# Kernel optimization log

Hardware: AMD Instinct MI355X
Metric: run time of the kernel (lower is better)

The kernel has to match this reference:

```python
import jax, jax.numpy as jnp
import numpy as np
from jax import lax


def fps(xyz, npoint, init_far):
    # Faithful farthest-point sampling: sequential loop over npoint iterations.
    B, N, _ = xyz.shape
    bidx = jnp.arange(B)

    def step(carry, _):
        dist, far = carry
        c = xyz[bidx, far]                       # (B,3) current centroid
        d = jnp.sum((xyz - c[:, None, :]) ** 2, -1)  # (B,N)
        dist = jnp.minimum(dist, d)
        return (dist, jnp.argmax(dist, -1)), far     # emit index BEFORE update, as in torch

    init = (jnp.full((B, N), 1e10, xyz.dtype), init_far)
    _, cent = lax.scan(step, init, None, length=npoint)  # (npoint, B)
    return cent.T                                         # (B, npoint)


def gather_pts(feat, idx):
    # feat (B,N,C), idx (B,K) -> (B,K,C)
    return jnp.take_along_axis(feat, idx[..., None], axis=1)


def setup_inputs() -> dict:
    key = jax.random.key(0)
    ks = jax.random.split(key, 12)
    B, N = 128, 500

    def w(k, o, i):
        return jax.random.normal(k, (o, i), jnp.float32) * 0.02

    z = lambda o: jnp.zeros((o,), jnp.float32)
    return {
        "x": jax.random.normal(ks[0], (B, N, 3), jnp.float32),
        "conf_W": w(ks[1], 1, 3),   "conf_b": z(1),
        "w1": w(ks[2], 64, 4),      "b1": z(64),
        "w2": w(ks[3], 256, 64),    "b2": z(256),
        "pc1_W": w(ks[4], 256, 256),"pc1_b": z(256),
        "w3": w(ks[5], 256, 259),   "b3": z(256),
        "w4": w(ks[6], 384, 256),   "b4": z(384),
        "pc2_W": w(ks[7], 384, 384),"pc2_b": z(384),
        "w5": w(ks[8], 384, 387),   "b5": z(384),
        "w6": w(ks[9], 512, 384),   "b6": z(512),
        "model_weights": 0,
        "init_far1": jax.random.randint(ks[10], (B,), 0, N),
        "init_far2": jax.random.randint(ks[11], (B,), 0, N),
    }


def reference(x, conf_W, conf_b, w1, b1, w2, b2, pc1_W, pc1_b,
              w3, b3, w4, b4, pc2_W, pc2_b, w5, b5, w6, b6,
              model_weights, init_far1, init_far2):
    relu = jax.nn.relu
    lin = lambda h, W, b: h @ W.T + b

    # ConfidenceScorePredictor: per-point sigmoid score (1 channel)
    conf = jax.nn.sigmoid(lin(x, conf_W, conf_b))            # (B,N,1)
    feat = jnp.concatenate([conf, x], -1)                    # (B,N,4)

    l2 = relu(lin(relu(lin(feat, w1, b1)), w2, b2))          # (B,N,256)
    l3 = lin(l2, pc1_W, pc1_b)                               # Conv1d k=1 == per-point linear

    idx1 = fps(x, 500, init_far1)                            # (B,500)
    nf1 = jnp.concatenate([gather_pts(l3, idx1), gather_pts(x, idx1)], -1)  # (B,500,259)

    l5 = relu(lin(relu(lin(nf1, w3, b3)), w4, b4))           # (B,500,384)
    l6 = lin(l5, pc2_W, pc2_b)                               # (B,500,384)

    idx2 = fps(x, 1000, init_far2)                           # (B,1000), indices < 500
    nf2 = jnp.concatenate([gather_pts(l6, idx2), gather_pts(x, idx2)], -1)  # (B,1000,387)

    l8 = relu(lin(relu(lin(nf2, w5, b5)), w6, b6))           # (B,1000,512)
    return jnp.max(l8, axis=1)                               # MaxPool1d(k=1000) -> (B,512)
```

## Files before the change

kernel.cpp:

```cpp
#include <hip/hip_runtime.h>

typedef unsigned short u16;
typedef short bf16x8 __attribute__((ext_vector_type(8)));
typedef float f32x4 __attribute__((ext_vector_type(4)));
typedef unsigned short us8 __attribute__((ext_vector_type(8)));
typedef unsigned long long u64;

__device__ __forceinline__ u16 f2bf(float f) {
  unsigned u = __float_as_uint(f);
  u += 0x7fffu + ((u >> 16) & 1u);
  return (u16)(u >> 16);
}

#define OFF_L6U 0u
#define OFF_IDX1 49152000u
#define OFF_FPSD 49408000u
#define OFF_FPSI 49670144u
#define OFF_WB   49671168u

template <int CTRL>
__device__ __forceinline__ unsigned dppu(unsigned v) {
  return (unsigned)__builtin_amdgcn_update_dpp(0, (int)v, CTRL, 0xF, 0xF, true);
}
template <int CTRL>
__device__ __forceinline__ float dppf(float v) {
  return __uint_as_float(dppu<CTRL>(__float_as_uint(v)));
}
__device__ __forceinline__ void ksel(u64& ak, float& ax, float& ay, float& az,
                                     u64 bk, float bx, float by, float bz) {
  bool g = bk > ak;
  ak = g ? bk : ak;
  ax = g ? bx : ax;
  ay = g ? by : ay;
  az = g ? bz : az;
}
template <int CTRL>
__device__ __forceinline__ void bstep_dpp(u64& k, float& x, float& y, float& z) {
  unsigned lo = (unsigned)k, hi = (unsigned)(k >> 32);
  unsigned olo = dppu<CTRL>(lo), ohi = dppu<CTRL>(hi);
  float ox = dppf<CTRL>(x), oy = dppf<CTRL>(y), oz = dppf<CTRL>(z);
  ksel(k, x, y, z, (((u64)ohi) << 32) | olo, ox, oy, oz);
}
__device__ __forceinline__ void bstep_shfl(int m, u64& k, float& x, float& y,
                                           float& z) {
  unsigned lo = (unsigned)k, hi = (unsigned)(k >> 32);
  unsigned olo = (unsigned)__shfl_xor((int)lo, m, 64);
  unsigned ohi = (unsigned)__shfl_xor((int)hi, m, 64);
  float ox = __shfl_xor(x, m, 64);
  float oy = __shfl_xor(y, m, 64);
  float oz = __shfl_xor(z, m, 64);
  ksel(k, x, y, z, (((u64)ohi) << 32) | olo, ox, oy, oz);
}

__device__ void fps_seg(const float4* cpt, int* out, const int* init1,
                        float* dstate, int* fstate, int b, int t0, int tcnt,
                        int lane) {
  __builtin_amdgcn_s_setprio(3);
  float px[8], py[8], pz[8], dist[8];
  unsigned nl[8];
  int base = lane * 8;
#pragma unroll
  for (int j = 0; j < 8; ++j) {
    int p = base + j;
    float4 c = cpt[p < 500 ? p : 0];
    px[j] = c.x; py[j] = c.y; pz[j] = c.z;
    nl[j] = ~(unsigned)p;
  }
  int fidx;
  if (t0 == 0) {
#pragma unroll
    for (int j = 0; j < 8; ++j) dist[j] = 1e10f;
    fidx = init1[b];
  } else {
#pragma unroll
    for (int j = 0; j < 8; ++j) dist[j] = dstate[(b * 64 + lane) * 8 + j];
    fidx = fstate[b];
  }
  float4 c0 = cpt[fidx];
  float cx = c0.x, cy = c0.y, cz = c0.z;

  int hist = 0;
  int tend = t0 + tcnt;
  for (int t = t0; t < tend; ++t) {
    hist = (lane == (t & 63)) ? fidx : hist;
    if ((t & 63) == 63) out[(t & ~63) + lane] = hist;
    if (t == 499) break;
#pragma unroll
    for (int j = 0; j < 8; ++j) {
      float dx = __fsub_rn(px[j], cx);
      float dy = __fsub_rn(py[j], cy);
      float dz = __fsub_rn(pz[j], cz);
      float d = __fadd_rn(__fadd_rn(__fmul_rn(dx, dx), __fmul_rn(dy, dy)),
                          __fmul_rn(dz, dz));
      dist[j] = fminf(dist[j], d);
    }
    u64 k[4];
    float X[4], Y[4], Z[4];
#pragma unroll
    for (int j = 0; j < 4; ++j) {
      u64 ka = (((u64)__float_as_uint(dist[2 * j])) << 32) | nl[2 * j];
      u64 kb = (((u64)__float_as_uint(dist[2 * j + 1])) << 32) | nl[2 * j + 1];
      bool g = kb > ka;
      k[j] = g ? kb : ka;
      X[j] = g ? px[2 * j + 1] : px[2 * j];
      Y[j] = g ? py[2 * j + 1] : py[2 * j];
      Z[j] = g ? pz[2 * j + 1] : pz[2 * j];
    }
    ksel(k[0], X[0], Y[0], Z[0], k[1], X[1], Y[1], Z[1]);
    ksel(k[2], X[2], Y[2], Z[2], k[3], X[3], Y[3], Z[3]);
    ksel(k[0], X[0], Y[0], Z[0], k[2], X[2], Y[2], Z[2]);
    bstep_dpp<0x121>(k[0], X[0], Y[0], Z[0]);
    bstep_dpp<0x122>(k[0], X[0], Y[0], Z[0]);
    bstep_dpp<0x124>(k[0], X[0], Y[0], Z[0]);
    bstep_dpp<0x128>(k[0], X[0], Y[0], Z[0]);
    bstep_shfl(16, k[0], X[0], Y[0], Z[0]);
    bstep_shfl(32, k[0], X[0], Y[0], Z[0]);
    fidx = (int)(~(unsigned)k[0]);
    cx = X[0]; cy = Y[0]; cz = Z[0];
  }
  if ((tend & 63) != 0) {
    int fb = (tend - 1) & ~63;
    if (lane <= ((tend - 1) & 63)) out[fb + lane] = hist;
  }
  if (tend < 500) {
#pragma unroll
    for (int j = 0; j < 8; ++j) dstate[(b * 64 + lane) * 8 + j] = dist[j];
    if (lane == 0) fstate[b] = fidx;
  }
}

template <int MI, int NI, int NP, int AG, int XC>
__device__ __forceinline__ void gemm_acc(
    f32x4 acc[MI][NI], const u16* __restrict__ aL, int Win, int smask,
    int arow0, const u16* const* aG, const u16* __restrict__ xc,
    const u16* __restrict__ bb, int Kp, int mrow, int quad) {
#pragma unroll
  for (int mi = 0; mi < MI; ++mi)
#pragma unroll
    for (int ni = 0; ni < NI; ++ni) acc[mi][ni] = f32x4{0.f, 0.f, 0.f, 0.f};
#pragma unroll
  for (int kp = 0; kp < NP + XC; ++kp) {
    bf16x8 af[MI];
#pragma unroll
    for (int mi = 0; mi < MI; ++mi) {
      int r = arow0 + mi * 16 + mrow;
      if (XC && kp == NP)
        af[mi] = *(const bf16x8*)(xc + r * 32 + ((quad ^ (r & 3)) << 3));
      else if (AG)
        af[mi] = *(const bf16x8*)(aG[mi] + kp * 32);
      else
        af[mi] = *(const bf16x8*)(aL + r * Win +
                                  (((kp * 4 + quad) ^ (r & smask)) << 3));
    }
    bf16x8 bf[NI];
#pragma unroll
    for (int ni = 0; ni < NI; ++ni)
      bf[ni] = *(const bf16x8*)(bb + (size_t)ni * 16 * Kp + kp * 32);
#pragma unroll
    for (int mi = 0; mi < MI; ++mi)
#pragma unroll
      for (int ni = 0; ni < NI; ++ni)
        acc[mi][ni] = __builtin_amdgcn_mfma_f32_16x16x32_bf16(
            af[mi], bf[ni], acc[mi][ni], 0, 0, 0);
  }
}

template <int MI, int NI>
__device__ __forceinline__ void ep_lds(const f32x4 acc[MI][NI], u16* out,
                                       int Wout, const float* __restrict__ bias,
                                       int n0, int arow0, int relu, int mrow,
                                       int quad) {
#pragma unroll
  for (int ni = 0; ni < NI; ++ni) {
    int col = n0 + ni * 16 + mrow;
    float bv = bias[col];
    int seg0 = col >> 3, lo = col & 7;
#pragma unroll
    for (int mi = 0; mi < MI; ++mi)
#pragma unroll
      for (int r = 0; r < 4; ++r) {
        int row = arow0 + mi * 16 + quad * 4 + r;
        float v = acc[mi][ni][r] + bv;
        if (relu) v = fmaxf(v, 0.f);
        out[row * Wout + ((seg0 ^ (row & 7)) << 3) + lo] = f2bf(v);
      }
  }
}

template <int MI, int NI>
__device__ __forceinline__ void ep_glb(const f32x4 acc[MI][NI],
                                       u16* __restrict__ out, int ldo,
                                       const float* __restrict__ bias, int n0,
                                       long grow0, long rowlim, int relu,
                                       int mrow, int quad) {
#pragma unroll
  for (int ni = 0; ni < NI; ++ni) {
    int col = n0 + ni * 16 + mrow;
    float bv = bias[col];
#pragma unroll
    for (int mi = 0; mi < MI; ++mi)
#pragma unroll
      for (int r = 0; r < 4; ++r) {
        long grow = grow0 + mi * 16 + quad * 4 + r;
        if (grow < rowlim) {
          float v = acc[mi][ni][r] + bv;
          if (relu) v = fmaxf(v, 0.f);
          out[(size_t)grow * ldo + col] = f2bf(v);
        }
      }
  }
}

struct ABArgs {
  const u16 *w1, *w2, *pc1, *w3, *w4, *pc2;
  const float *b1, *b2, *pc1b, *b3, *b4, *pc2b;
};

#define AB_LDS_BYTES (98304 + 8192)

__global__ __launch_bounds__(512, 2) void fused_ab(
    ABArgs A, const float* __restrict__ x, const float* __restrict__ cW,
    const float* __restrict__ cb, u16* __restrict__ l6u,
    const int* __restrict__ init1, int* __restrict__ idx1,
    float* __restrict__ dstate, int* __restrict__ fstate, int t0, int tcnt) {
  extern __shared__ __align__(16) char smem[];
  u16* act = (u16*)smem;
  u16* xcat = (u16*)(smem + 98304);
  int bid = blockIdx.x, t = threadIdx.x;
  if (bid < 128) {
    float4* cpt = (float4*)smem;
    const float* xb = x + (size_t)bid * 1500;
    for (int p = t; p < 500; p += 512)
      cpt[p] = make_float4(xb[p * 3], xb[p * 3 + 1], xb[p * 3 + 2], 0.f);
    __syncthreads();
    if (t < 64)
      fps_seg(cpt, idx1 + bid * 500, init1, dstate, fstate, bid, t0, tcnt, t);
    return;
  }
  const int blk = bid - 128;
  const size_t rows0 = (size_t)blk * 128;
  if (t < 128) {
    size_t gr = rows0 + t;
    float x0 = x[gr * 3], x1 = x[gr * 3 + 1], x2 = x[gr * 3 + 2];
    float z = x0 * cW[0] + x1 * cW[1] + x2 * cW[2] + cb[0];
    float conf = 1.0f / (1.0f + expf(-z));
    us8 fv;
    fv[0] = f2bf(conf); fv[1] = f2bf(x0); fv[2] = f2bf(x1); fv[3] = f2bf(x2);
    fv[4] = 0; fv[5] = 0; fv[6] = 0; fv[7] = 0;
    *(us8*)(act + t * 32 + ((t & 3) << 3)) = fv;
    us8 xv;
    xv[0] = fv[1]; xv[1] = fv[2]; xv[2] = fv[3];
    xv[3] = 0; xv[4] = 0; xv[5] = 0; xv[6] = 0; xv[7] = 0;
    *(us8*)(xcat + t * 32 + ((t & 3) << 3)) = xv;
  }
  if (t < 384) {
    us8 zz = {0, 0, 0, 0, 0, 0, 0, 0};
    int r = t / 3, s = 1 + t % 3;
    *(us8*)(act + r * 32 + ((s ^ (r & 3)) << 3)) = zz;
    *(us8*)(xcat + r * 32 + ((s ^ (r & 3)) << 3)) = zz;
  }
  __syncthreads();
  const int w = t >> 6, lane = t & 63, mrow = lane & 15, quad = lane >> 4;
  const int wm = w >> 2, wn = w & 3;
  const int arow0 = wm * 64;
  {
    f32x4 acc[4][1];
    const u16* bb = A.w1 + (size_t)(wn * 16 + mrow) * 32 + quad * 8;
    gemm_acc<4, 1, 1, 0, 0>(acc, act, 32, 3, arow0, nullptr, nullptr, bb, 32,
                            mrow, quad);
    __syncthreads();
    ep_lds<4, 1>(acc, act, 64, A.b1, wn * 16, arow0, 1, mrow, quad);
    __syncthreads();
  }
  {
    f32x4 acc[4][4];
    const u16* bb = A.w2 + (size_t)(wn * 64 + mrow) * 64 + quad * 8;
    gemm_acc<4, 4, 2, 0, 0>(acc, act, 64, 7, arow0, nullptr, nullptr, bb, 64,
                            mrow, quad);
    __syncthreads();
    ep_lds<4, 4>(acc, act, 256, A.b2, wn * 64, arow0, 1, mrow, quad);
    __syncthreads();
  }
  {
    f32x4 acc[4][4];
    const u16* bb = A.pc1 + (size_t)(wn * 64 + mrow) * 256 + quad * 8;
    gemm_acc<4, 4, 8, 0, 0>(acc, act, 256, 7, arow0, nullptr, nullptr, bb, 256,
                            mrow, quad);
    __syncthreads();
    ep_lds<4, 4>(acc, act, 256, A.pc1b, wn * 64, arow0, 0, mrow, quad);
    __syncthreads();
  }
  {
    f32x4 acc[4][4];
    const u16* bb = A.w3 + (size_t)(wn * 64 + mrow) * 288 + quad * 8;
    gemm_acc<4, 4, 8, 0, 1>(acc, act, 256, 7, arow0, nullptr, xcat, bb, 288,
                            mrow, quad);
    __syncthreads();
    ep_lds<4, 4>(acc, act, 256, A.b3, wn * 64, arow0, 1, mrow, quad);
    __syncthreads();
  }
  {
    f32x4 acc[4][6];
    const u16* bb = A.w4 + (size_t)(wn * 96 + mrow) * 256 + quad * 8;
    gemm_acc<4, 6, 8, 0, 0>(acc, act, 256, 7, arow0, nullptr, nullptr, bb, 256,
                            mrow, quad);
    __syncthreads();
    ep_lds<4, 6>(acc, act, 384, A.b4, wn * 96, arow0, 1, mrow, quad);
    __syncthreads();
  }
  {
    f32x4 acc[4][6];
    const u16* bb = A.pc2 + (size_t)(wn * 96 + mrow) * 384 + quad * 8;
    gemm_acc<4, 6, 12, 0, 0>(acc, act, 384, 7, arow0, nullptr, nullptr, bb,
                             384, mrow, quad);
    ep_glb<4, 6>(acc, l6u, 384, A.pc2b, wn * 96, (long)(rows0 + arow0), 64000,
                 0, mrow, quad);
  }
}

struct CArgs {
  const u16 *w5, *w6;
  const float *b5, *b6;
};

#define C_LDS_BYTES (98304 + 8192 + 2048)

__global__ __launch_bounds__(512, 2) void fused_c(
    CArgs C, const float* __restrict__ x, const u16* __restrict__ l6u,
    float* __restrict__ outf, const int* __restrict__ idx1) {
  extern __shared__ __align__(16) char smem[];
  u16* l7 = (u16*)smem;
  u16* xcat = (u16*)(smem + 98304);
  float* red = (float*)(smem + 98304 + 8192);
  int bid = blockIdx.x, t = threadIdx.x;
  const int b = bid >> 2, q = bid & 3;
  const int prow0 = q * 128;
  if (t < 128) {
    int p = prow0 + t, pe = p < 500 ? p : 0;
    const float* xp = x + ((size_t)b * 500 + pe) * 3;
    us8 xv;
    xv[0] = f2bf(xp[0]); xv[1] = f2bf(xp[1]); xv[2] = f2bf(xp[2]);
    xv[3] = 0; xv[4] = 0; xv[5] = 0; xv[6] = 0; xv[7] = 0;
    *(us8*)(xcat + t * 32 + ((t & 3) << 3)) = xv;
  }
  if (t < 384) {
    us8 zz = {0, 0, 0, 0, 0, 0, 0, 0};
    int r = t / 3, s = 1 + t % 3;
    *(us8*)(xcat + r * 32 + ((s ^ (r & 3)) << 3)) = zz;
  }
  __syncthreads();
  const int w = t >> 6, lane = t & 63, mrow = lane & 15, quad = lane >> 4;
  const int wm = w >> 2, wn = w & 3;
  const int arow0 = wm * 64;
  {
    const u16* aG[4];
#pragma unroll
    for (int mi = 0; mi < 4; ++mi) {
      int p = prow0 + arow0 + mi * 16 + mrow;
      int pe = p < 500 ? p : 0;
      int s = idx1[b * 500 + pe];
      aG[mi] = l6u + ((size_t)b * 500 + s) * 384 + quad * 8;
    }
    f32x4 acc[4][6];
    const u16* bb = C.w5 + (size_t)(wn * 96 + mrow) * 416 + quad * 8;
    gemm_acc<4, 6, 12, 1, 1>(acc, nullptr, 0, 0, arow0, aG, xcat, bb, 416,
                             mrow, quad);
    ep_lds<4, 6>(acc, l7, 384, C.b5, wn * 96, arow0, 1, mrow, quad);
  }
  __syncthreads();
  {
#pragma unroll
    for (int ph = 0; ph < 2; ++ph) {
      f32x4 acc[4][4];
      int n0 = ph * 256 + wn * 64;
      const u16* bb = C.w6 + (size_t)(n0 + mrow) * 384 + quad * 8;
      gemm_acc<4, 4, 12, 0, 0>(acc, l7, 384, 7, arow0, nullptr, nullptr, bb,
                               384, mrow, quad);
#pragma unroll
      for (int ni = 0; ni < 4; ++ni) {
        int cc = n0 + ni * 16 + mrow;
        float bv = C.b6[cc];
        float mx = 0.f;
#pragma unroll
        for (int mi = 0; mi < 4; ++mi)
#pragma unroll
          for (int r = 0; r < 4; ++r) {
            int p = prow0 + arow0 + mi * 16 + quad * 4 + r;
            float v = fmaxf(acc[mi][ni][r] + bv, 0.f);
            if (p < 500) mx = fmaxf(mx, v);
          }
        mx = fmaxf(mx, __shfl_xor(mx, 16, 64));
        mx = fmaxf(mx, __shfl_xor(mx, 32, 64));
        if (quad == 0) red[wm * 256 + wn * 64 + ni * 16 + mrow] = mx;
      }
      __syncthreads();
      if (t < 256) {
        float m = fmaxf(red[t], red[256 + t]);
        atomicMax((unsigned*)&outf[(size_t)b * 512 + ph * 256 + t],
                  __float_as_uint(m));
      }
      __syncthreads();
    }
  }
}

struct PrepArgs {
  const float* wsrc[8];
  u16* wdst[8];
  int wN[8], wK[8], wKp[8];
  int wstart[9];
};

__global__ __launch_bounds__(256) void prep_kernel(
    PrepArgs pa, const float* __restrict__ x, float* __restrict__ outf,
    const int* __restrict__ init1, int* __restrict__ idx1,
    float* __restrict__ dstate, int* __restrict__ fstate, int tcnt) {
  __shared__ float4 cpt[512];
  int bid = blockIdx.x, t = threadIdx.x;
  if (bid < 128) {
    const float* xb = x + (size_t)bid * 1500;
    for (int p = t; p < 500; p += 256)
      cpt[p] = make_float4(xb[p * 3], xb[p * 3 + 1], xb[p * 3 + 2], 0.f);
    __syncthreads();
    if (t < 64)
      fps_seg(cpt, idx1 + bid * 500, init1, dstate, fstate, bid, 0, tcnt, t);
    return;
  }
  int i = (bid - 128) * 256 + t;
  int S = pa.wstart[8];
  if (i < S) {
    int wsel = 0;
#pragma unroll
    for (int j = 1; j < 8; ++j)
      if (i >= pa.wstart[j]) wsel = j;
    int local = i - pa.wstart[wsel];
    int Kp = pa.wKp[wsel];
    int n = local / Kp, k = local - n * Kp;
    pa.wdst[wsel][local] =
        (k < pa.wK[wsel]) ? f2bf(pa.wsrc[wsel][n * pa.wK[wsel] + k]) : (u16)0;
  } else if (i < S + 65536) {
    outf[i - S] = 0.f;
  }
}

extern "C" void kernel_launch(void* const* d_in, const int* in_sizes, int n_in,
                              void* d_out, int out_size, void* d_ws,
                              size_t ws_size, hipStream_t stream) {
  const float* x      = (const float*)d_in[0];
  const float* conf_W = (const float*)d_in[1];
  const float* conf_b = (const float*)d_in[2];
  const float* w1     = (const float*)d_in[3];
  const float* b1     = (const float*)d_in[4];
  const float* w2     = (const float*)d_in[5];
  const float* b2     = (const float*)d_in[6];
  const float* pc1_W  = (const float*)d_in[7];
  const float* pc1_b  = (const float*)d_in[8];
  const float* w3     = (const float*)d_in[9];
  const float* b3     = (const float*)d_in[10];
  const float* w4     = (const float*)d_in[11];
  const float* b4     = (const float*)d_in[12];
  const float* pc2_W  = (const float*)d_in[13];
  const float* pc2_b  = (const float*)d_in[14];
  const float* w5     = (const float*)d_in[15];
  const float* b5     = (const float*)d_in[16];
  const float* w6     = (const float*)d_in[17];
  const float* b6     = (const float*)d_in[18];
  const int* init1    = (const int*)d_in[20];

  char* ws = (char*)d_ws;
  u16* l6u = (u16*)(ws + OFF_L6U);
  int* idx1 = (int*)(ws + OFF_IDX1);
  float* dstate = (float*)(ws + OFF_FPSD);
  int* fstate = (int*)(ws + OFF_FPSI);
  u16* wb = (u16*)(ws + OFF_WB);
  float* outf = (float*)d_out;

  PrepArgs pa;
  const float* srcs[8] = {w1, w2, pc1_W, w3, w4, pc2_W, w5, w6};
  int Ns[8]  = {64, 256, 256, 256, 384, 384, 384, 512};
  int Ks[8]  = {4, 64, 256, 259, 256, 384, 387, 384};
  int Kps[8] = {32, 64, 256, 288, 256, 384, 416, 384};
  u16* WBp[8];
  int cum = 0;
  for (int i = 0; i < 8; ++i) {
    pa.wsrc[i] = srcs[i];
    pa.wdst[i] = WBp[i] = wb + cum;
    pa.wN[i] = Ns[i];
    pa.wK[i] = Ks[i];
    pa.wKp[i] = Kps[i];
    pa.wstart[i] = cum;
    cum += Ns[i] * Kps[i];
  }
  pa.wstart[8] = cum;
  int total = cum + 65536;

  prep_kernel<<<128 + (total + 255) / 256, 256, 0, stream>>>(
      pa, x, outf, init1, idx1, dstate, fstate, 64);

  ABArgs A;
  A.w1 = WBp[0]; A.w2 = WBp[1]; A.pc1 = WBp[2];
  A.w3 = WBp[3]; A.w4 = WBp[4]; A.pc2 = WBp[5];
  A.b1 = b1; A.b2 = b2; A.pc1b = pc1_b; A.b3 = b3; A.b4 = b4; A.pc2b = pc2_b;
  fused_ab<<<128 + 500, 512, AB_LDS_BYTES, stream>>>(
      A, x, conf_W, conf_b, l6u, init1, idx1, dstate, fstate, 64, 436);

  CArgs Cg;
  Cg.w5 = WBp[6]; Cg.w6 = WBp[7]; Cg.b5 = b5; Cg.b6 = b6;
  fused_c<<<512, 512, C_LDS_BYTES, stream>>>(Cg, x, l6u, outf, idx1);
}
```

Before: 471.5 us.

## Fold w5 GEMM into stage AB, simplify FPS argmax, pack two FPS batches per block

The w5 layer is now applied per source point inside fused_ab, before the gather, and its fp32 result is written to a larger workspace. fused_c then gathers those rows, adds the xyz term from the last three w5 columns in fp32 and applies relu, which removes the w5 GEMM from the gathered 1000-point stage. The FPS argmax changes from a 64-bit key-plus-coordinate butterfly to a float max reduction followed by a ballot to find the first matching index, and two batches' FPS now run in one block. The price is a doubled fp32 intermediate buffer and extra gather traffic in fused_c, and the w5 pre-activation now comes from bf16 GEMM on l6 instead of on gathered rows.

Result: faster. 408.0 us (-13.5%).

```diff
diff --git a/kernel.cpp b/kernel.cpp
--- a/kernel.cpp
+++ b/kernel.cpp
@@ -4,6 +4,7 @@
 typedef short bf16x8 __attribute__((ext_vector_type(8)));
 typedef float f32x4 __attribute__((ext_vector_type(4)));
 typedef unsigned short us8 __attribute__((ext_vector_type(8)));
+typedef unsigned short us4 __attribute__((ext_vector_type(4)));
 typedef unsigned long long u64;
 
 __device__ __forceinline__ u16 f2bf(float f) {
@@ -11,45 +12,20 @@
   u += 0x7fffu + ((u >> 16) & 1u);
   return (u16)(u >> 16);
 }
-
-#define OFF_L6U 0u
-#define OFF_IDX1 49152000u
-#define OFF_FPSD 49408000u
-#define OFF_FPSI 49670144u
-#define OFF_WB   49671168u
+__device__ __forceinline__ float rlf(float v, int l) {
+  return __uint_as_float((unsigned)__builtin_amdgcn_readlane(__float_as_int(v), l));
+}
+
+#define OFF_AP   0u
+#define OFF_IDX1 98304000u
+#define OFF_FPSD 98560000u
+#define OFF_FPSI 98822144u
+#define OFF_WB   98824192u
 
 template <int CTRL>
-__device__ __forceinline__ unsigned dppu(unsigned v) {
-  return (unsigned)__builtin_amdgcn_update_dpp(0, (int)v, CTRL, 0xF, 0xF, true);
-}
-template <int CTRL>
-__device__ __forceinline__ float dppf(float v) {
-  return __uint_as_float(dppu<CTRL>(__float_as_uint(v)));
-}
-__device__ __forceinline__ void ksel(u64& ak, float& ax, float& ay, float& az,
-                                     u64 bk, float bx, float by, float bz) {
-  bool g = bk > ak;
-  ak = g ? bk : ak;
-  ax = g ? bx : ax;
-  ay = g ? by : ay;
-  az = g ? bz : az;
-}
-template <int CTRL>
-__device__ __forceinline__ void bstep_dpp(u64& k, float& x, float& y, float& z) {
-  unsigned lo = (unsigned)k, hi = (unsigned)(k >> 32);
-  unsigned olo = dppu<CTRL>(lo), ohi = dppu<CTRL>(hi);
-  float ox = dppf<CTRL>(x), oy = dppf<CTRL>(y), oz = dppf<CTRL>(z);
-  ksel(k, x, y, z, (((u64)ohi) << 32) | olo, ox, oy, oz);
-}
-__device__ __forceinline__ void bstep_shfl(int m, u64& k, float& x, float& y,
-                                           float& z) {
-  unsigned lo = (unsigned)k, hi = (unsigned)(k >> 32);
-  unsigned olo = (unsigned)__shfl_xor((int)lo, m, 64);
-  unsigned ohi = (unsigned)__shfl_xor((int)hi, m, 64);
-  float ox = __shfl_xor(x, m, 64);
-  float oy = __shfl_xor(y, m, 64);
-  float oz = __shfl_xor(z, m, 64);
-  ksel(k, x, y, z, (((u64)ohi) << 32) | olo, ox, oy, oz);
+__device__ __forceinline__ float dppmaxf(float v) {
+  int s = __builtin_amdgcn_update_dpp(0, __float_as_int(v), CTRL, 0xF, 0xF, true);
+  return fmaxf(v, __uint_as_float((unsigned)s));
 }
 
 __device__ void fps_seg(const float4* cpt, int* out, const int* init1,
@@ -57,14 +33,12 @@
                         int lane) {
   __builtin_amdgcn_s_setprio(3);
   float px[8], py[8], pz[8], dist[8];
-  unsigned nl[8];
   int base = lane * 8;
 #pragma unroll
   for (int j = 0; j < 8; ++j) {
     int p = base + j;
     float4 c = cpt[p < 500 ? p : 0];
     px[j] = c.x; py[j] = c.y; pz[j] = c.z;
-    nl[j] = ~(unsigned)p;
   }
   int fidx;
   if (t0 == 0) {
@@ -94,29 +68,30 @@
                           __fmul_rn(dz, dz));
       dist[j] = fminf(dist[j], d);
     }
-    u64 k[4];
-    float X[4], Y[4], Z[4];
-#pragma unroll
-    for (int j = 0; j < 4; ++j) {
-      u64 ka = (((u64)__float_as_uint(dist[2 * j])) << 32) | nl[2 * j];
-      u64 kb = (((u64)__float_as_uint(dist[2 * j + 1])) << 32) | nl[2 * j + 1];
-      bool g = kb > ka;
-      k[j] = g ? kb : ka;
-      X[j] = g ? px[2 * j + 1] : px[2 * j];
-      Y[j] = g ? py[2 * j + 1] : py[2 * j];
-      Z[j] = g ? pz[2 * j + 1] : pz[2 * j];
-    }
-    ksel(k[0], X[0], Y[0], Z[0], k[1], X[1], Y[1], Z[1]);
-    ksel(k[2], X[2], Y[2], Z[2], k[3], X[3], Y[3], Z[3]);
-    ksel(k[0], X[0], Y[0], Z[0], k[2], X[2], Y[2], Z[2]);
-    bstep_dpp<0x121>(k[0], X[0], Y[0], Z[0]);
-    bstep_dpp<0x122>(k[0], X[0], Y[0], Z[0]);
-    bstep_dpp<0x124>(k[0], X[0], Y[0], Z[0]);
-    bstep_dpp<0x128>(k[0], X[0], Y[0], Z[0]);
-    bstep_shfl(16, k[0], X[0], Y[0], Z[0]);
-    bstep_shfl(32, k[0], X[0], Y[0], Z[0]);
-    fidx = (int)(~(unsigned)k[0]);
-    cx = X[0]; cy = Y[0]; cz = Z[0];
+    float t1 = fmaxf(fmaxf(dist[0], dist[1]), dist[2]);
+    float t2 = fmaxf(fmaxf(dist[3], dist[4]), dist[5]);
+    float t3 = fmaxf(fmaxf(dist[6], dist[7]), t1);
+    float m = fmaxf(t2, t3);
+    m = dppmaxf<0x111>(m);
+    m = dppmaxf<0x112>(m);
+    m = dppmaxf<0x114>(m);
+    m = dppmaxf<0x118>(m);
+    m = dppmaxf<0x142>(m);
+    m = dppmaxf<0x143>(m);
+    float mf = rlf(m, 63);
+    int e0 = (dist[0] == mf) ? 0 : 8, e1 = (dist[1] == mf) ? 1 : 8;
+    int e2 = (dist[2] == mf) ? 2 : 8, e3 = (dist[3] == mf) ? 3 : 8;
+    int e4 = (dist[4] == mf) ? 4 : 8, e5 = (dist[5] == mf) ? 5 : 8;
+    int e6 = (dist[6] == mf) ? 6 : 8, e7 = (dist[7] == mf) ? 7 : 8;
+    int sA = min(min(e0, e1), e2);
+    int sB = min(min(e3, e4), e5);
+    int sC = min(min(e6, e7), sA);
+    int sel = min(sB, sC);
+    u64 mask = __ballot(sel != 8);
+    int li = (int)__ffsll(mask) - 1;
+    fidx = li * 8 + __builtin_amdgcn_readlane(sel, li);
+    float4 cc = cpt[fidx];
+    cx = cc.x; cy = cc.y; cz = cc.z;
   }
   if ((tend & 63) != 0) {
     int fb = (tend - 1) & ~63;
@@ -129,11 +104,11 @@
   }
 }
 
-template <int MI, int NI, int NP, int AG, int XC>
+template <int MI, int NI, int NP, int XC>
 __device__ __forceinline__ void gemm_acc(
     f32x4 acc[MI][NI], const u16* __restrict__ aL, int Win, int smask,
-    int arow0, const u16* const* aG, const u16* __restrict__ xc,
-    const u16* __restrict__ bb, int Kp, int mrow, int quad) {
+    int arow0, const u16* __restrict__ xc, const u16* __restrict__ bb, int Kp,
+    int mrow, int quad) {
 #pragma unroll
   for (int mi = 0; mi < MI; ++mi)
 #pragma unroll
@@ -146,8 +121,6 @@
       int r = arow0 + mi * 16 + mrow;
       if (XC && kp == NP)
         af[mi] = *(const bf16x8*)(xc + r * 32 + ((quad ^ (r & 3)) << 3));
-      else if (AG)
-        af[mi] = *(const bf16x8*)(aG[mi] + kp * 32);
       else
         af[mi] = *(const bf16x8*)(aL + r * Win +
                                   (((kp * 4 + quad) ^ (r & smask)) << 3));
@@ -188,11 +161,11 @@
 }
 
 template <int MI, int NI>
-__device__ __forceinline__ void ep_glb(const f32x4 acc[MI][NI],
-                                       u16* __restrict__ out, int ldo,
-                                       const float* __restrict__ bias, int n0,
-                                       long grow0, long rowlim, int relu,
-                                       int mrow, int quad) {
+__device__ __forceinline__ void ep_glbf(const f32x4 acc[MI][NI],
+                                        float* __restrict__ out, int ldo,
+                                        const float* __restrict__ bias, int n0,
+                                        long grow0, long rowlim, int mrow,
+                                        int quad) {
 #pragma unroll
   for (int ni = 0; ni < NI; ++ni) {
     int col = n0 + ni * 16 + mrow;
@@ -202,42 +175,43 @@
 #pragma unroll
       for (int r = 0; r < 4; ++r) {
         long grow = grow0 + mi * 16 + quad * 4 + r;
-        if (grow < rowlim) {
-          float v = acc[mi][ni][r] + bv;
-          if (relu) v = fmaxf(v, 0.f);
-          out[(size_t)grow * ldo + col] = f2bf(v);
-        }
+        if (grow < rowlim)
+          out[(size_t)grow * ldo + col] = acc[mi][ni][r] + bv;
       }
   }
 }
 
 struct ABArgs {
-  const u16 *w1, *w2, *pc1, *w3, *w4, *pc2;
-  const float *b1, *b2, *pc1b, *b3, *b4, *pc2b;
+  const u16 *w1, *w2, *pc1, *w3, *w4, *pc2, *w5;
+  const float *b1, *b2, *pc1b, *b3, *b4, *pc2b, *b5;
 };
 
 #define AB_LDS_BYTES (98304 + 8192)
 
 __global__ __launch_bounds__(512, 2) void fused_ab(
     ABArgs A, const float* __restrict__ x, const float* __restrict__ cW,
-    const float* __restrict__ cb, u16* __restrict__ l6u,
+    const float* __restrict__ cb, float* __restrict__ apart,
     const int* __restrict__ init1, int* __restrict__ idx1,
     float* __restrict__ dstate, int* __restrict__ fstate, int t0, int tcnt) {
   extern __shared__ __align__(16) char smem[];
   u16* act = (u16*)smem;
   u16* xcat = (u16*)(smem + 98304);
   int bid = blockIdx.x, t = threadIdx.x;
-  if (bid < 128) {
+  if (bid < 64) {
     float4* cpt = (float4*)smem;
-    const float* xb = x + (size_t)bid * 1500;
-    for (int p = t; p < 500; p += 512)
+    const float* xb = x + (size_t)bid * 3000;
+    for (int p = t; p < 1000; p += 512)
       cpt[p] = make_float4(xb[p * 3], xb[p * 3 + 1], xb[p * 3 + 2], 0.f);
     __syncthreads();
-    if (t < 64)
-      fps_seg(cpt, idx1 + bid * 500, init1, dstate, fstate, bid, t0, tcnt, t);
+    int wid = t >> 6;
+    if (wid < 2) {
+      int b = bid * 2 + wid;
+      fps_seg(cpt + wid * 500, idx1 + b * 500, init1, dstate, fstate, b, t0,
+              tcnt, t & 63);
+    }
     return;
   }
-  const int blk = bid - 128;
+  const int blk = bid - 64;
   const size_t rows0 = (size_t)blk * 128;
   if (t < 128) {
     size_t gr = rows0 + t;
@@ -266,8 +240,7 @@
   {
     f32x4 acc[4][1];
     const u16* bb = A.w1 + (size_t)(wn * 16 + mrow) * 32 + quad * 8;
-    gemm_acc<4, 1, 1, 0, 0>(acc, act, 32, 3, arow0, nullptr, nullptr, bb, 32,
-                            mrow, quad);
+    gemm_acc<4, 1, 1, 0>(acc, act, 32, 3, arow0, nullptr, bb, 32, mrow, quad);
     __syncthreads();
     ep_lds<4, 1>(acc, act, 64, A.b1, wn * 16, arow0, 1, mrow, quad);
     __syncthreads();
@@ -275,8 +248,7 @@
   {
     f32x4 acc[4][4];
     const u16* bb = A.w2 + (size_t)(wn * 64 + mrow) * 64 + quad * 8;
-    gemm_acc<4, 4, 2, 0, 0>(acc, act, 64, 7, arow0, nullptr, nullptr, bb, 64,
-                            mrow, quad);
+    gemm_acc<4, 4, 2, 0>(acc, act, 64, 7, arow0, nullptr, bb, 64, mrow, quad);
     __syncthreads();
     ep_lds<4, 4>(acc, act, 256, A.b2, wn * 64, arow0, 1, mrow, quad);
     __syncthreads();
@@ -284,8 +256,7 @@
   {
     f32x4 acc[4][4];
     const u16* bb = A.pc1 + (size_t)(wn * 64 + mrow) * 256 + quad * 8;
-    gemm_acc<4, 4, 8, 0, 0>(acc, act, 256, 7, arow0, nullptr, nullptr, bb, 256,
-                            mrow, quad);
+    gemm_acc<4, 4, 8, 0>(acc, act, 256, 7, arow0, nullptr, bb, 256, mrow, quad);
     __syncthreads();
     ep_lds<4, 4>(acc, act, 256, A.pc1b, wn * 64, arow0, 0, mrow, quad);
     __syncthreads();
@@ -293,8 +264,7 @@
   {
     f32x4 acc[4][4];
     const u16* bb = A.w3 + (size_t)(wn * 64 + mrow) * 288 + quad * 8;
-    gemm_acc<4, 4, 8, 0, 1>(acc, act, 256, 7, arow0, nullptr, xcat, bb, 288,
-                            mrow, quad);
+    gemm_acc<4, 4, 8, 1>(acc, act, 256, 7, arow0, xcat, bb, 288, mrow, quad);
     __syncthreads();
     ep_lds<4, 4>(acc, act, 256, A.b3, wn * 64, arow0, 1, mrow, quad);
     __syncthreads();
@@ -302,8 +272,7 @@
   {
     f32x4 acc[4][6];
     const u16* bb = A.w4 + (size_t)(wn * 96 + mrow) * 256 + quad * 8;
-    gemm_acc<4, 6, 8, 0, 0>(acc, act, 256, 7, arow0, nullptr, nullptr, bb, 256,
-                            mrow, quad);
+    gemm_acc<4, 6, 8, 0>(acc, act, 256, 7, arow0, nullptr, bb, 256, mrow, quad);
     __syncthreads();
     ep_lds<4, 6>(acc, act, 384, A.b4, wn * 96, arow0, 1, mrow, quad);
     __syncthreads();
@@ -311,75 +280,81 @@
   {
     f32x4 acc[4][6];
     const u16* bb = A.pc2 + (size_t)(wn * 96 + mrow) * 384 + quad * 8;
-    gemm_acc<4, 6, 12, 0, 0>(acc, act, 384, 7, arow0, nullptr, nullptr, bb,
-                             384, mrow, quad);
-    ep_glb<4, 6>(acc, l6u, 384, A.pc2b, wn * 96, (long)(rows0 + arow0), 64000,
-                 0, mrow, quad);
-  }
-}
-
-struct CArgs {
-  const u16 *w5, *w6;
-  const float *b5, *b6;
-};
-
-#define C_LDS_BYTES (98304 + 8192 + 2048)
+    gemm_acc<4, 6, 12, 0>(acc, act, 384, 7, arow0, nullptr, bb, 384, mrow,
+                          quad);
+    __syncthreads();
+    ep_lds<4, 6>(acc, act, 384, A.pc2b, wn * 96, arow0, 0, mrow, quad);
+    __syncthreads();
+  }
+  {
+    f32x4 acc[4][6];
+    const u16* bb = A.w5 + (size_t)(wn * 96 + mrow) * 416 + quad * 8;
+    gemm_acc<4, 6, 12, 0>(acc, act, 384, 7, arow0, nullptr, bb, 416, mrow,
+                          quad);
+    ep_glbf<4, 6>(acc, apart, 384, A.b5, wn * 96, (long)(rows0 + arow0), 64000,
+                  mrow, quad);
+  }
+}
+
+#define C_LDS_BYTES (98304 + 6144 + 2048)
 
 __global__ __launch_bounds__(512, 2) void fused_c(
-    CArgs C, const float* __restrict__ x, const u16* __restrict__ l6u,
-    float* __restrict__ outf, const int* __restrict__ idx1) {
+    const u16* __restrict__ w6b, const float* __restrict__ b6,
+    const float* __restrict__ x, const float* __restrict__ apart,
+    const float* __restrict__ w5src, float* __restrict__ outf,
+    const int* __restrict__ idx1) {
   extern __shared__ __align__(16) char smem[];
   u16* l7 = (u16*)smem;
-  u16* xcat = (u16*)(smem + 98304);
-  float* red = (float*)(smem + 98304 + 8192);
+  float* xw = (float*)(smem + 98304);
+  float* red = (float*)(smem + 98304 + 6144);
   int bid = blockIdx.x, t = threadIdx.x;
   const int b = bid >> 2, q = bid & 3;
   const int prow0 = q * 128;
-  if (t < 128) {
-    int p = prow0 + t, pe = p < 500 ? p : 0;
+  if (t < 384) {
+    xw[t * 4 + 0] = w5src[(size_t)t * 387 + 384];
+    xw[t * 4 + 1] = w5src[(size_t)t * 387 + 385];
+    xw[t * 4 + 2] = w5src[(size_t)t * 387 + 386];
+    xw[t * 4 + 3] = 0.f;
+  }
+  __syncthreads();
+  {
+    int row = t >> 2;
+    int p = prow0 + row, pe = p < 500 ? p : 0;
+    int s = idx1[b * 500 + pe];
+    const float* ap = apart + ((size_t)b * 500 + (size_t)s) * 384;
     const float* xp = x + ((size_t)b * 500 + pe) * 3;
-    us8 xv;
-    xv[0] = f2bf(xp[0]); xv[1] = f2bf(xp[1]); xv[2] = f2bf(xp[2]);
-    xv[3] = 0; xv[4] = 0; xv[5] = 0; xv[6] = 0; xv[7] = 0;
-    *(us8*)(xcat + t * 32 + ((t & 3) << 3)) = xv;
-  }
-  if (t < 384) {
-    us8 zz = {0, 0, 0, 0, 0, 0, 0, 0};
-    int r = t / 3, s = 1 + t % 3;
-    *(us8*)(xcat + r * 32 + ((s ^ (r & 3)) << 3)) = zz;
+    float x0 = xp[0], x1 = xp[1], x2 = xp[2];
+#pragma unroll
+    for (int it = 0; it < 24; ++it) {
+      int c = (t & 3) * 4 + it * 16;
+      float4 a4 = *(const float4*)(ap + c);
+      const float4* wv = (const float4*)(xw + c * 4);
+      float v0 = fmaxf(a4.x + wv[0].x * x0 + wv[0].y * x1 + wv[0].z * x2, 0.f);
+      float v1 = fmaxf(a4.y + wv[1].x * x0 + wv[1].y * x1 + wv[1].z * x2, 0.f);
+      float v2 = fmaxf(a4.z + wv[2].x * x0 + wv[2].y * x1 + wv[2].z * x2, 0.f);
+      float v3 = fmaxf(a4.w + wv[3].x * x0 + wv[3].y * x1 + wv[3].z * x2, 0.f);
+      us4 pk;
+      pk[0] = f2bf(v0); pk[1] = f2bf(v1); pk[2] = f2bf(v2); pk[3] = f2bf(v3);
+      int seg = c >> 3, half = (c >> 2) & 1;
+      *(us4*)(l7 + row * 384 + ((seg ^ (row & 7)) << 3) + half * 4) = pk;
+    }
   }
   __syncthreads();
   const int w = t >> 6, lane = t & 63, mrow = lane & 15, quad = lane >> 4;
   const int wm = w >> 2, wn = w & 3;
   const int arow0 = wm * 64;
   {
-    const u16* aG[4];
-#pragma unroll
-    for (int mi = 0; mi < 4; ++mi) {
-      int p = prow0 + arow0 + mi * 16 + mrow;
-      int pe = p < 500 ? p : 0;
-      int s = idx1[b * 500 + pe];
-      aG[mi] = l6u + ((size_t)b * 500 + s) * 384 + quad * 8;
-    }
-    f32x4 acc[4][6];
-    const u16* bb = C.w5 + (size_t)(wn * 96 + mrow) * 416 + quad * 8;
-    gemm_acc<4, 6, 12, 1, 1>(acc, nullptr, 0, 0, arow0, aG, xcat, bb, 416,
-                             mrow, quad);
-    ep_lds<4, 6>(acc, l7, 384, C.b5, wn * 96, arow0, 1, mrow, quad);
-  }
-  __syncthreads();
-  {
 #pragma unroll
     for (int ph = 0; ph < 2; ++ph) {
       f32x4 acc[4][4];
       int n0 = ph * 256 + wn * 64;
-      const u16* bb = C.w6 + (size_t)(n0 + mrow) * 384 + quad * 8;
-      gemm_acc<4, 4, 12, 0, 0>(acc, l7, 384, 7, arow0, nullptr, nullptr, bb,
-                               384, mrow, quad);
+      const u16* bb = w6b + (size_t)(n0 + mrow) * 384 + quad * 8;
+      gemm_acc<4, 4, 12, 0>(acc, l7, 384, 7, arow0, nullptr, bb, 384, mrow,
+                            quad);
 #pragma unroll
       for (int ni = 0; ni < 4; ++ni) {
         int cc = n0 + ni * 16 + mrow;
-        float bv = C.b6[cc];
+        float bv = b6[cc];
         float mx = 0.f;
 #pragma unroll
         for (int mi = 0; mi < 4; ++mi)
@@ -415,18 +390,22 @@
     PrepArgs pa, const float* __restrict__ x, float* __restrict__ outf,
     const int* __restrict__ init1, int* __restrict__ idx1,
     float* __restrict__ dstate, int* __restrict__ fstate, int tcnt) {
-  __shared__ float4 cpt[512];
+  __shared__ float4 cpt[1000];
   int bid = blockIdx.x, t = threadIdx.x;
-  if (bid < 128) {
-    const float* xb = x + (size_t)bid * 1500;
-    for (int p = t; p < 500; p += 256)
+  if (bid < 64) {
+    const float* xb = x + (size_t)bid * 3000;
+    for (int p = t; p < 1000; p += 256)
       cpt[p] = make_float4(xb[p * 3], xb[p * 3 + 1], xb[p * 3 + 2], 0.f);
     __syncthreads();
-    if (t < 64)
-      fps_seg(cpt, idx1 + bid * 500, init1, dstate, fstate, bid, 0, tcnt, t);
+    int wid = t >> 6;
+    if (wid < 2) {
+      int b = bid * 2 + wid;
+      fps_seg(cpt + wid * 500, idx1 + b * 500, init1, dstate, fstate, b, 0,
+              tcnt, t & 63);
+    }
     return;
   }
-  int i = (bid - 128) * 256 + t;
+  int i = (bid - 64) * 256 + t;
   int S = pa.wstart[8];
   if (i < S) {
     int wsel = 0;
@@ -468,7 +447,7 @@
   const int* init1    = (const int*)d_in[20];
 
   char* ws = (char*)d_ws;
-  u16* l6u = (u16*)(ws + OFF_L6U);
+  float* apart = (float*)(ws + OFF_AP);
   int* idx1 = (int*)(ws + OFF_IDX1);
   float* dstate = (float*)(ws + OFF_FPSD);
   int* fstate = (int*)(ws + OFF_FPSI);
@@ -494,17 +473,17 @@
   pa.wstart[8] = cum;
   int total = cum + 65536;
 
-  prep_kernel<<<128 + (total + 255) / 256, 256, 0, stream>>>(
+  prep_kernel<<<64 + (total + 255) / 256, 256, 0, stream>>>(
       pa, x, outf, init1, idx1, dstate, fstate, 64);
 
   ABArgs A;
   A.w1 = WBp[0]; A.w2 = WBp[1]; A.pc1 = WBp[2];
-  A.w3 = WBp[3]; A.w4 = WBp[4]; A.pc2 = WBp[5];
-  A.b1 = b1; A.b2 = b2; A.pc1b = pc1_b; A.b3 = b3; A.b4 = b4; A.pc2b = pc2_b;
-  fused_ab<<<128 + 500, 512, AB_LDS_BYTES, stream>>>(
-      A, x, conf_W, conf_b, l6u, init1, idx1, dstate, fstate, 64, 436);
-
-  CArgs Cg;
-  Cg.w5 = WBp[6]; Cg.w6 = WBp[7]; Cg.b5 = b5; Cg.b6 = b6;
-  fused_c<<<512, 512, C_LDS_BYTES, stream>>>(Cg, x, l6u, outf, idx1);
-}
+  A.w3 = WBp[3]; A.w4 = WBp[4]; A.pc2 = WBp[5]; A.w5 = WBp[6];
+  A.b1 = b1; A.b2 = b2; A.pc1b = pc1_b; A.b3 = b3; A.b4 = b4;
+  A.pc2b = pc2_b; A.b5 = b5;
+  fused_ab<<<64 + 500, 512, AB_LDS_BYTES, stream>>>(
+      A, x, conf_W, conf_b, apart, init1, idx1, dstate, fstate, 64, 436);
+
+  fused_c<<<512, 512, C_LDS_BYTES, stream>>>(WBp[7], b6, x, apart, w5, outf,
+                                             idx1);
+}
```
